# Optimization experiments

Measured on AMD Instinct MI355X. Metric: run time of the kernel, lower is better.

The kernel has to match this reference:

```python
import jax, jax.numpy as jnp
import numpy as np


def setup_inputs() -> dict:
    key = jax.random.key(0)
    k1, k2 = jax.random.split(key)
    shape = (16, 64, 32, 28, 28)  # (b, c, t, h, w)
    x = jax.random.normal(k1, shape, dtype=jnp.float32)
    x_v = jax.random.normal(k2, shape, dtype=jnp.float32)
    return {"x": x, "x_v": x_v}


def reference(x, x_v):
    b, c, t, h, w = x.shape
    d = c * h * w
    # (b, t, d): flatten channel+spatial into feature dim per frame
    r_q = jnp.transpose(x, (0, 2, 1, 3, 4)).reshape(b, t, d)
    r_v = jnp.transpose(x_v, (0, 2, 1, 3, 4)).reshape(b, t, d)
    # (b, t, t) frame-frame similarity
    m_t = jnp.einsum('bqd,bkd->bqk', r_q, r_q)
    # NOTE: softmax over the BATCH axis (dim=0), faithful to the original
    m_t = jax.nn.softmax(m_t, axis=0)
    a_t = jnp.einsum('bqk,bkd->bqd', m_t, r_v)
    a = a_t.reshape(b, t, c, h, w).transpose(0, 2, 1, 3, 4)
    return a
```

## Files before the change

### kernel.cpp

```cpp
#include <hip/hip_runtime.h>

namespace {

constexpr int Tt = 32;
constexpr int Ss = 784;

using bf16x8 = __attribute__((ext_vector_type(8))) short;
using f32x4  = __attribute__((ext_vector_type(4))) float;

__device__ inline void cvt2(float a, float b, unsigned& h, unsigned& l) {
  const unsigned ha = __float_as_uint(a) >> 16;
  const unsigned hb = __float_as_uint(b) >> 16;
  const float ra = a - __uint_as_float(ha << 16);
  const float rb = b - __uint_as_float(hb << 16);
  const unsigned la = __float_as_uint(ra) >> 16;
  const unsigned lb = __float_as_uint(rb) >> 16;
  h = ha | (hb << 16);
  l = la | (lb << 16);
}

__global__ __launch_bounds__(256, 3) void gram_partial(const float* __restrict__ x,
                                                       float* __restrict__ part) {
  const int bc = blockIdx.x;
  const float* __restrict__ xb = x + (size_t)bc * (Tt * Ss);
  const int tid  = threadIdx.x;
  const int w    = tid >> 6;
  const int lane = tid & 63;

  __shared__ uint4 HI[13 * 128];
  __shared__ uint4 LO[13 * 128];

  f32x4 d1[2][2], d2[2][2], d3[2][2];
#pragma unroll
  for (int i = 0; i < 2; ++i)
#pragma unroll
    for (int j = 0; j < 2; ++j) { d1[i][j] = 0.f; d2[i][j] = 0.f; d3[i][j] = 0.f; }

  const int fbase = ((lane >> 4) << 5) + (lane & 15);

#pragma unroll
  for (int phase = 0; phase < 2; ++phase) {
    const int sb  = phase ? 416 : 0;
    const int nks = phase ? 12 : 13;

    for (int f = tid; f < nks * 128; f += 256) {
      const int ks  = f >> 7;
      const int idx = f & 127;
      const int kg  = idx >> 5;
      const int row = idx & 31;
      const int s   = sb + ks * 32 + kg * 8;
      uint4 h = {0u, 0u, 0u, 0u}, l = {0u, 0u, 0u, 0u};
      if (s < 784) {
        const float* p = xb + row * Ss + s;
        const float4 v0 = *reinterpret_cast<const float4*>(p);
        const float4 v1 = *reinterpret_cast<const float4*>(p + 4);
        cvt2(v0.x, v0.y, h.x, l.x);
        cvt2(v0.z, v0.w, h.y, l.y);
        cvt2(v1.x, v1.y, h.z, l.z);
        cvt2(v1.z, v1.w, h.w, l.w);
      }
      HI[f] = h;
      LO[f] = l;
    }
    __syncthreads();

    for (int ks = w; ks < nks; ks += 4) {
      const int base = ks * 128 + fbase;
      const uint4 h0u = HI[base], h1u = HI[base + 16];
      const uint4 l0u = LO[base], l1u = LO[base + 16];
      const bf16x8 h0 = __builtin_bit_cast(bf16x8, h0u);
      const bf16x8 h1 = __builtin_bit_cast(bf16x8, h1u);
      const bf16x8 l0 = __builtin_bit_cast(bf16x8, l0u);
      const bf16x8 l1 = __builtin_bit_cast(bf16x8, l1u);
      d1[0][0] = __builtin_amdgcn_mfma_f32_16x16x32_bf16(h0, h0, d1[0][0], 0, 0, 0);
      d1[0][1] = __builtin_amdgcn_mfma_f32_16x16x32_bf16(h0, h1, d1[0][1], 0, 0, 0);
      d1[1][0] = __builtin_amdgcn_mfma_f32_16x16x32_bf16(h1, h0, d1[1][0], 0, 0, 0);
      d1[1][1] = __builtin_amdgcn_mfma_f32_16x16x32_bf16(h1, h1, d1[1][1], 0, 0, 0);
      d2[0][0] = __builtin_amdgcn_mfma_f32_16x16x32_bf16(h0, l0, d2[0][0], 0, 0, 0);
      d2[0][1] = __builtin_amdgcn_mfma_f32_16x16x32_bf16(h0, l1, d2[0][1], 0, 0, 0);
      d2[1][0] = __builtin_amdgcn_mfma_f32_16x16x32_bf16(h1, l0, d2[1][0], 0, 0, 0);
      d2[1][1] = __builtin_amdgcn_mfma_f32_16x16x32_bf16(h1, l1, d2[1][1], 0, 0, 0);
      d3[0][0] = __builtin_amdgcn_mfma_f32_16x16x32_bf16(l0, h0, d3[0][0], 0, 0, 0);
      d3[0][1] = __builtin_amdgcn_mfma_f32_16x16x32_bf16(l0, h1, d3[0][1], 0, 0, 0);
      d3[1][0] = __builtin_amdgcn_mfma_f32_16x16x32_bf16(l1, h0, d3[1][0], 0, 0, 0);
      d3[1][1] = __builtin_amdgcn_mfma_f32_16x16x32_bf16(l1, h1, d3[1][1], 0, 0, 0);
    }
    __syncthreads();
  }

  float* mtmp = reinterpret_cast<float*>(HI);
#pragma unroll
  for (int i = 0; i < 2; ++i)
#pragma unroll
    for (int j = 0; j < 2; ++j) {
      const f32x4 s4 = d1[i][j] + d2[i][j] + d3[i][j];
#pragma unroll
      for (int r = 0; r < 4; ++r) {
        const int row = i * 16 + ((lane >> 4) << 2) + r;
        const int col = j * 16 + (lane & 15);
        mtmp[w * 1056 + row * 33 + col] = s4[r];
      }
    }
  __syncthreads();

  const int e0 = tid * 4;
  float tmp[4];
#pragma unroll
  for (int u = 0; u < 4; ++u) {
    const int row = (e0 + u) >> 5;
    const int col = (e0 + u) & 31;
    float ss = 0.f;
#pragma unroll
    for (int ww = 0; ww < 4; ++ww) ss += mtmp[ww * 1056 + row * 33 + col];
    tmp[u] = ss;
  }
  float4 o4;
  o4.x = tmp[0]; o4.y = tmp[1]; o4.z = tmp[2]; o4.w = tmp[3];
  *reinterpret_cast<float4*>(part + (size_t)bc * 1024 + e0) = o4;
}

__global__ __launch_bounds__(256) void reduce_c(const float* __restrict__ part,
                                                float* __restrict__ msum) {
  const int bid = blockIdx.x;
  const int b   = bid >> 2;
  const int e   = (bid & 3) * 256 + threadIdx.x;
  const float* __restrict__ p = part + (size_t)b * 64 * 1024 + e;
  float s0 = 0.f, s1 = 0.f, s2 = 0.f, s3 = 0.f;
#pragma unroll
  for (int c = 0; c < 64; c += 4) {
    s0 += p[(size_t)(c + 0) * 1024];
    s1 += p[(size_t)(c + 1) * 1024];
    s2 += p[(size_t)(c + 2) * 1024];
    s3 += p[(size_t)(c + 3) * 1024];
  }
  msum[b * 1024 + e] = (s0 + s1) + (s2 + s3);
}

__global__ __launch_bounds__(256) void softmax_b(const float* __restrict__ msum,
                                                 float* __restrict__ mt) {
  const int e = blockIdx.x * 256 + threadIdx.x;
  float l[16];
  float mx = -3.4e38f;
#pragma unroll
  for (int b = 0; b < 16; ++b) {
    l[b] = msum[b * 1024 + e];
    mx = fmaxf(mx, l[b]);
  }
  float s = 0.f;
#pragma unroll
  for (int b = 0; b < 16; ++b) {
    l[b] = expf(l[b] - mx);
    s += l[b];
  }
  const float inv = 1.f / s;
  const int et = (e & 31) * 32 + (e >> 5);
#pragma unroll
  for (int b = 0; b < 16; ++b) mt[b * 1024 + et] = l[b] * inv;
}

__global__ __launch_bounds__(256) void pv(const float* __restrict__ xv,
                                          const float* __restrict__ mt,
                                          float* __restrict__ out) {
  const int gbl   = blockIdx.x;
  const int bc    = gbl >> 2;
  const int chunk = gbl & 3;
  const int b     = bc >> 6;
  const float* __restrict__ xvb = xv + (size_t)bc * (Tt * Ss) + chunk * 196;
  float* __restrict__ ob        = out + (size_t)bc * (Tt * Ss) + chunk * 196;

  const int tid  = threadIdx.x;
  const int w    = tid >> 6;
  const int lane = tid & 63;
  const int q0   = __builtin_amdgcn_readfirstlane(8 * w);
  const int moff = __builtin_amdgcn_readfirstlane(b * 1024 + q0);
  const float* __restrict__ mrow = mt + moff;

  if (lane < 49) {
    const float* __restrict__ src = xvb + 4 * lane;
    float4 acc[8] = {};
    float4 va[4], vb4[4];
#pragma unroll
    for (int t = 0; t < 4; ++t)
      va[t] = *reinterpret_cast<const float4*>(src + (size_t)t * Ss);

#pragma unroll
    for (int kc = 0; kc < 4; ++kc) {
#pragma unroll
      for (int t = 0; t < 4; ++t)
        vb4[t] = *reinterpret_cast<const float4*>(src + (size_t)(8 * kc + 4 + t) * Ss);
#pragma unroll
      for (int t = 0; t < 4; ++t) {
        const int k = 8 * kc + t;
#pragma unroll
        for (int r = 0; r < 8; ++r) {
          const float m = mrow[k * 32 + r];
          acc[r].x += m * va[t].x; acc[r].y += m * va[t].y;
          acc[r].z += m * va[t].z; acc[r].w += m * va[t].w;
        }
      }
      if (kc < 3) {
#pragma unroll
        for (int t = 0; t < 4; ++t)
          va[t] = *reinterpret_cast<const float4*>(src + (size_t)(8 * kc + 8 + t) * Ss);
      }
#pragma unroll
      for (int t = 0; t < 4; ++t) {
        const int k = 8 * kc + 4 + t;
#pragma unroll
        for (int r = 0; r < 8; ++r) {
          const float m = mrow[k * 32 + r];
          acc[r].x += m * vb4[t].x; acc[r].y += m * vb4[t].y;
          acc[r].z += m * vb4[t].z; acc[r].w += m * vb4[t].w;
        }
      }
    }

#pragma unroll
    for (int r = 0; r < 8; ++r)
      *reinterpret_cast<float4*>(ob + (size_t)(q0 + r) * Ss + 4 * lane) = acc[r];
  }
}

}

extern "C" void kernel_launch(void* const* d_in, const int* in_sizes, int n_in,
                              void* d_out, int out_size, void* d_ws, size_t ws_size,
                              hipStream_t stream) {
  const float* x  = (const float*)d_in[0];
  const float* xv = (const float*)d_in[1];
  float* out = (float*)d_out;

  float* part = (float*)d_ws;
  float* msum = part + 1024 * 1024;
  float* mt   = msum + 16 * 1024;

  gram_partial<<<dim3(1024), dim3(256), 0, stream>>>(x, part);
  reduce_c<<<dim3(64), dim3(256), 0, stream>>>(part, msum);
  softmax_b<<<dim3(4), dim3(256), 0, stream>>>(msum, mt);
  pv<<<dim3(4096), dim3(256), 0, stream>>>(xv, mt, out);
}
```

Measured before the change: 87.87 us.

## Restructure pv kernel to one block per (b,c) with 8-wide per-lane tiles

The PV kernel now launches one 512-thread block per (batch, channel) instead of four 256-thread blocks per slice. Each lane handles 8 spatial elements instead of 4, loading the softmax weights as two float4 vector loads per k rather than scalar loads. The manual double-buffered prefetch is replaced by a simple k loop unrolled by 2. The aim is fewer blocks, wider per-thread reuse of the weights and vectorised weight loads, at the cost of more accumulator registers (64 floats) and less explicit latency hiding.

Measured after the change: 108.7 us. 23.7% more time.

```diff
diff --git a/kernel.cpp b/kernel.cpp
--- a/kernel.cpp
+++ b/kernel.cpp
@@ -158,66 +158,47 @@
   for (int b = 0; b < 16; ++b) mt[b * 1024 + et] = l[b] * inv;
 }
 
-__global__ __launch_bounds__(256) void pv(const float* __restrict__ xv,
-                                          const float* __restrict__ mt,
-                                          float* __restrict__ out) {
-  const int gbl   = blockIdx.x;
-  const int bc    = gbl >> 2;
-  const int chunk = gbl & 3;
-  const int b     = bc >> 6;
-  const float* __restrict__ xvb = xv + (size_t)bc * (Tt * Ss) + chunk * 196;
-  float* __restrict__ ob        = out + (size_t)bc * (Tt * Ss) + chunk * 196;
-
+__global__ __launch_bounds__(512, 4) void pv(const float* __restrict__ xv,
+                                             const float* __restrict__ mt,
+                                             float* __restrict__ out) {
+  const int bc = blockIdx.x;
+  const int b  = bc >> 6;
   const int tid  = threadIdx.x;
   const int w    = tid >> 6;
   const int lane = tid & 63;
-  const int q0   = __builtin_amdgcn_readfirstlane(8 * w);
-  const int moff = __builtin_amdgcn_readfirstlane(b * 1024 + q0);
-  const float* __restrict__ mrow = mt + moff;
+  const int q0    = 8 * (w & 3);
+  const int sbase = 392 * (w >> 2);
+
+  const float* __restrict__ mp = mt + b * 1024 + q0;
 
   if (lane < 49) {
-    const float* __restrict__ src = xvb + 4 * lane;
-    float4 acc[8] = {};
-    float4 va[4], vb4[4];
-#pragma unroll
-    for (int t = 0; t < 4; ++t)
-      va[t] = *reinterpret_cast<const float4*>(src + (size_t)t * Ss);
-
-#pragma unroll
-    for (int kc = 0; kc < 4; ++kc) {
-#pragma unroll
-      for (int t = 0; t < 4; ++t)
-        vb4[t] = *reinterpret_cast<const float4*>(src + (size_t)(8 * kc + 4 + t) * Ss);
-#pragma unroll
-      for (int t = 0; t < 4; ++t) {
-        const int k = 8 * kc + t;
-#pragma unroll
-        for (int r = 0; r < 8; ++r) {
-          const float m = mrow[k * 32 + r];
-          acc[r].x += m * va[t].x; acc[r].y += m * va[t].y;
-          acc[r].z += m * va[t].z; acc[r].w += m * va[t].w;
-        }
+    const float* __restrict__ src = xv + (size_t)bc * (Tt * Ss) + sbase + 8 * lane;
+    float* __restrict__ dst       = out + (size_t)bc * (Tt * Ss) + sbase + 8 * lane;
+
+    float4 acc[8][2] = {};
+
+#pragma unroll 2
+    for (int k = 0; k < 32; ++k) {
+      const float4 v0 = *reinterpret_cast<const float4*>(src + (size_t)k * Ss);
+      const float4 v1 = *reinterpret_cast<const float4*>(src + (size_t)k * Ss + 4);
+      const float4 ma = *reinterpret_cast<const float4*>(mp + k * 32);
+      const float4 mb = *reinterpret_cast<const float4*>(mp + k * 32 + 4);
+      const float mm[8] = {ma.x, ma.y, ma.z, ma.w, mb.x, mb.y, mb.z, mb.w};
+#pragma unroll
+      for (int r = 0; r < 8; ++r) {
+        const float m = mm[r];
+        acc[r][0].x += m * v0.x; acc[r][0].y += m * v0.y;
+        acc[r][0].z += m * v0.z; acc[r][0].w += m * v0.w;
+        acc[r][1].x += m * v1.x; acc[r][1].y += m * v1.y;
+        acc[r][1].z += m * v1.z; acc[r][1].w += m * v1.w;
       }
-      if (kc < 3) {
-#pragma unroll
-        for (int t = 0; t < 4; ++t)
-          va[t] = *reinterpret_cast<const float4*>(src + (size_t)(8 * kc + 8 + t) * Ss);
-      }
-#pragma unroll
-      for (int t = 0; t < 4; ++t) {
-        const int k = 8 * kc + 4 + t;
-#pragma unroll
-        for (int r = 0; r < 8; ++r) {
-          const float m = mrow[k * 32 + r];
-          acc[r].x += m * vb4[t].x; acc[r].y += m * vb4[t].y;
-          acc[r].z += m * vb4[t].z; acc[r].w += m * vb4[t].w;
-        }
-      }
-    }
-
-#pragma unroll
-    for (int r = 0; r < 8; ++r)
-      *reinterpret_cast<float4*>(ob + (size_t)(q0 + r) * Ss + 4 * lane) = acc[r];
+    }
+
+#pragma unroll
+    for (int r = 0; r < 8; ++r) {
+      *reinterpret_cast<float4*>(dst + (size_t)(q0 + r) * Ss)     = acc[r][0];
+      *reinterpret_cast<float4*>(dst + (size_t)(q0 + r) * Ss + 4) = acc[r][1];
+    }
   }
 }
 
@@ -237,5 +218,5 @@
   gram_partial<<<dim3(1024), dim3(256), 0, stream>>>(x, part);
   reduce_c<<<dim3(64), dim3(256), 0, stream>>>(part, msum);
   softmax_b<<<dim3(4), dim3(256), 0, stream>>>(msum, mt);
-  pv<<<dim3(4096), dim3(256), 0, stream>>>(xv, mt, out);
-}
+  pv<<<dim3(1024), dim3(512), 0, stream>>>(xv, mt, out);
+}
```
